# Performance work log

Measured on AMD Instinct MI355X. Metric: run time of the kernel, lower is better.

## Reference

```python
import jax, jax.numpy as jnp
import numpy as np
from jax import lax

DIM = 512
HEADS = 8
B, H, W = 8, 64, 64
EPS = 1e-12  # F.normalize default eps


def pointwise(x, w):
    # 1x1 conv, no bias: [B,C,H,W] x [O,C] -> [B,O,H,W]
    return jnp.einsum('oc,bchw->bohw', w, x)


def depthwise3x3(x, dw):
    # groups=C depthwise 3x3 conv, padding=1, no bias. dw: [C,1,3,3]
    return lax.conv_general_dilated(
        x, dw, window_strides=(1, 1), padding=((1, 1), (1, 1)),
        feature_group_count=x.shape[1],
        dimension_numbers=('NCHW', 'OIHW', 'NCHW'))


def setup_inputs() -> dict:
    key = jax.random.key(0)
    ks = jax.random.split(key, 8)
    s = 1.0 / np.sqrt(DIM)
    return {
        'x': jax.random.normal(ks[0], (B, DIM, H, W), jnp.float32),
        'w_q': jax.random.normal(ks[1], (DIM, DIM), jnp.float32) * s,
        'w_k': jax.random.normal(ks[2], (DIM, DIM), jnp.float32) * s,
        'w_v': jax.random.normal(ks[3], (DIM, DIM), jnp.float32) * s,
        'dw_q': jax.random.normal(ks[4], (DIM, 1, 3, 3), jnp.float32) * (1.0 / 3.0),
        'dw_k': jax.random.normal(ks[5], (DIM, 1, 3, 3), jnp.float32) * (1.0 / 3.0),
        'dw_v': jax.random.normal(ks[6], (DIM, 1, 3, 3), jnp.float32) * (1.0 / 3.0),
        'w_proj': jax.random.normal(ks[7], (DIM, DIM), jnp.float32) * s,
        'temperature': jnp.ones((HEADS, 1, 1), jnp.float32),
    }


def reference(x, w_q, w_k, w_v, dw_q, dw_k, dw_v, w_proj, temperature):
    b, c, h, w = x.shape
    d = c // HEADS
    hw = h * w

    q = depthwise3x3(pointwise(x, w_q), dw_q)
    k = depthwise3x3(pointwise(x, w_k), dw_k)
    v = depthwise3x3(pointwise(x, w_v), dw_v)

    # b (h d) x y -> b h d (x y)
    q = q.reshape(b, HEADS, d, hw)
    k = k.reshape(b, HEADS, d, hw)
    v = v.reshape(b, HEADS, d, hw)

    # L2-normalize over spatial axis (F.normalize, eps=1e-12)
    q = q / jnp.maximum(jnp.linalg.norm(q, axis=-1, keepdims=True), EPS)
    k = k / jnp.maximum(jnp.linalg.norm(k, axis=-1, keepdims=True), EPS)

    # channel attention: [b,h,d,d]
    attn = jnp.einsum('bhdn,bhen->bhde', q, k) * temperature
    attn = jax.nn.softmax(attn, axis=-1)
    out = jnp.einsum('bhde,bhen->bhdn', attn, v)  # [b,h,d,hw]

    out = out.reshape(b, c, h, w)
    return pointwise(out, w_proj)
```

## Files before the change

kernel.cpp:

```cpp
#include <hip/hip_runtime.h>
#include <hip/hip_bf16.h>
#include <stdint.h>

#define DEV __device__ __forceinline__

typedef __attribute__((ext_vector_type(8))) short   s16x8;
typedef __attribute__((ext_vector_type(8))) __bf16  bf16x8;
typedef __attribute__((ext_vector_type(4))) float   f32x4;

static constexpr int BATCH = 8;
static constexpr int DIM   = 512;
static constexpr int HEADS = 8;
static constexpr int HD    = 64;
static constexpr int HW    = 4096;
static constexpr int CQKV  = 1536;
static constexpr int NSPLIT = 8;

DEV void gload16(const void* g, void* l) {
  __builtin_amdgcn_global_load_lds(
      (const __attribute__((address_space(1))) void*)g,
      (__attribute__((address_space(3))) void*)l,
      16, 0, 0);
}

DEV f32x4 mfma16x32(s16x8 a, s16x8 b, f32x4 c) {
  return __builtin_amdgcn_mfma_f32_16x16x32_bf16(
      __builtin_bit_cast(bf16x8, a), __builtin_bit_cast(bf16x8, b), c, 0, 0, 0);
}

DEV float b2f(short x) {
  unsigned u = (unsigned)(unsigned short)x << 16;
  return __uint_as_float(u);
}
DEV short f2b(float f) { return __builtin_bit_cast(short, __float2bfloat16(f)); }

__global__ __launch_bounds__(256) void prep_weights(
    const float* __restrict__ wq, const float* __restrict__ wk,
    const float* __restrict__ wv, const float* __restrict__ wp,
    __hip_bfloat16* __restrict__ wqkv, __hip_bfloat16* __restrict__ wpb)
{
  int i = blockIdx.x * 256 + threadIdx.x;
  if (i < CQKV * DIM) {
    int r = i / DIM;
    const float* src = (r < 512) ? wq : (r < 1024) ? wk : wv;
    wqkv[i] = __float2bfloat16(src[(r & 511) * DIM + (i % DIM)]);
  } else {
    int j = i - CQKV * DIM;
    wpb[j] = __float2bfloat16(wp[j]);
  }
}

__global__ __launch_bounds__(256) void transpose_x(
    const float* __restrict__ x, __hip_bfloat16* __restrict__ XT)
{
  __shared__ float tile[64 * 65];
  const int n0 = blockIdx.x * 64, c0 = blockIdx.y * 64, b = blockIdx.z;
  const int t = threadIdx.x;
#pragma unroll
  for (int i = 0; i < 16; ++i) {
    int f = i * 256 + t; int ci = f >> 6, nj = f & 63;
    tile[ci * 65 + nj] = x[((long)b * DIM + c0 + ci) * HW + n0 + nj];
  }
  __syncthreads();
#pragma unroll
  for (int i = 0; i < 16; ++i) {
    int f = i * 256 + t; int ni = f >> 6, cj = f & 63;
    XT[((long)b * HW + n0 + ni) * DIM + c0 + cj] = __float2bfloat16(tile[cj * 65 + ni]);
  }
}

template <bool OUT_BF16>
__global__ __launch_bounds__(512, 2) void gemm_bt8(
    const __hip_bfloat16* __restrict__ A,
    const __hip_bfloat16* __restrict__ Bt,
    void* __restrict__ Cout,
    int M, int N, int K, long bt_bstride, long c_bstride)
{
  __shared__ __hip_bfloat16 lds[65536];
  const int t = threadIdx.x, w = t >> 6, l = t & 63;
  const int wm = w >> 2, wn = w & 3;
  const int m0 = blockIdx.y * 256, n0 = blockIdx.x * 256, b = blockIdx.z;
  const __hip_bfloat16* Bb = Bt + (long)b * bt_bstride;

  const int rl = t >> 3;
  const int ch = ((t & 7) ^ (rl & 7)) * 8;
  const int fr = l & 15, fk = (l >> 4) * 8;
  const int fswz = (l & 7) << 3;

  auto stageA = [&](int p, int h, int u) {
    const __hip_bfloat16* src = A + (long)(m0 + h * 64 + rl) * K + u * 64 + ch;
    __hip_bfloat16* dst = lds + p * 16384 + h * 8192 + w * 512;
    gload16(src, dst);
    gload16(src + 128l * K, dst + 4096);
  };
  auto stageB = [&](int p, int hb, int u) {
    const __hip_bfloat16* src = Bb + (long)(n0 + hb * 128 + rl) * K + u * 64 + ch;
    __hip_bfloat16* dst = lds + 32768 + p * 16384 + hb * 8192 + w * 512;
    gload16(src, dst);
    gload16(src + 64l * K, dst + 4096);
  };

  f32x4 acc[8][4] = {};
  const int NT = K >> 6;

  stageB(0, 0, 0); stageB(0, 1, 0); stageA(0, 0, 0); stageA(0, 1, 0);
  stageB(1, 0, 1); stageB(1, 1, 1); stageA(1, 0, 1);
  asm volatile("s_waitcnt vmcnt(6)" ::: "memory");
  __builtin_amdgcn_s_barrier();

  for (int u = 0; u < NT; ++u) {
    const int p = u & 1;
    const __hip_bfloat16* lA = lds + p * 16384 + wm * 4096;
    const __hip_bfloat16* lB = lds + 32768 + p * 16384 + (wn >> 1) * 8192
                             + (wn & 1) * 4096;
    s16x8 bfr[2][4];
#pragma unroll
    for (int q = 0; q < 4; ++q) {
      s16x8 afr[2][2];
#pragma unroll
      for (int kk = 0; kk < 2; ++kk)
#pragma unroll
        for (int mi = 0; mi < 2; ++mi)
          afr[kk][mi] = *(const s16x8*)&lA[(q >> 1) * 8192
              + ((q & 1) * 32 + mi * 16 + fr) * 64 + ((kk * 32 + fk) ^ fswz)];
      if (q == 0) {
#pragma unroll
        for (int kk = 0; kk < 2; ++kk)
#pragma unroll
          for (int ni = 0; ni < 4; ++ni)
            bfr[kk][ni] = *(const s16x8*)&lB[(ni * 16 + fr) * 64
                + ((kk * 32 + fk) ^ fswz)];
      }
      if (q == 0)      { if (u + 1 < NT) stageA(p ^ 1, 1, u + 1); }
      else if (q == 1) { if (u + 2 < NT) stageB(p, 0, u + 2); }
      else if (q == 2) { if (u + 2 < NT) stageB(p, 1, u + 2); }
      else {
        if (u + 2 < NT) stageA(p, 0, u + 2);
        if (u == NT - 2) asm volatile("s_waitcnt vmcnt(0)" ::: "memory");
        else             asm volatile("s_waitcnt vmcnt(6)" ::: "memory");
      }
      __builtin_amdgcn_s_barrier();
      asm volatile("s_waitcnt lgkmcnt(0)" ::: "memory");
      __builtin_amdgcn_sched_barrier(0);
      __builtin_amdgcn_s_setprio(1);
#pragma unroll
      for (int kk = 0; kk < 2; ++kk)
#pragma unroll
        for (int mi = 0; mi < 2; ++mi)
#pragma unroll
          for (int ni = 0; ni < 4; ++ni)
            acc[q * 2 + mi][ni] = mfma16x32(afr[kk][mi], bfr[kk][ni],
                                            acc[q * 2 + mi][ni]);
      __builtin_amdgcn_s_setprio(0);
      __builtin_amdgcn_s_barrier();
    }
  }

  const int row0 = m0 + wm * 128, col0 = n0 + wn * 64;
#pragma unroll
  for (int mi = 0; mi < 8; ++mi)
#pragma unroll
    for (int ni = 0; ni < 4; ++ni)
#pragma unroll
      for (int j = 0; j < 4; ++j) {
        long rr = row0 + mi * 16 + (l >> 4) * 4 + j;
        long cc = col0 + ni * 16 + fr;
        float v = acc[mi][ni][j];
        if (OUT_BF16)
          ((__hip_bfloat16*)Cout)[(long)b * c_bstride + rr * N + cc] = __float2bfloat16(v);
        else
          ((float*)Cout)[(long)b * c_bstride + rr * N + cc] = v;
      }
}

__global__ __launch_bounds__(256) void dwconv(
    __hip_bfloat16* __restrict__ P,
    const float* __restrict__ dwq, const float* __restrict__ dwk,
    const float* __restrict__ dwv, float* __restrict__ rnorm)
{
  __shared__ float pl[66 * 67];
  __shared__ float red4[4];
  const int c = blockIdx.x, b = blockIdx.y, t = threadIdx.x;
  const int w = t >> 6, l = t & 63;

  if (t < 66) { pl[t] = 0.f; pl[65 * 67 + t] = 0.f; }
  if (t >= 128 && t < 192) { pl[(t - 127) * 67] = 0.f; }
  if (t >= 192)            { pl[(t - 191) * 67 + 65] = 0.f; }

  const long base = ((long)b * CQKV + c) * HW;
  const int y = t >> 2, x0 = (t & 3) * 16;
  s16x8 v0 = *(const s16x8*)&P[base + t * 16];
  s16x8 v1 = *(const s16x8*)&P[base + t * 16 + 8];
#pragma unroll
  for (int j = 0; j < 8; ++j) {
    pl[(y + 1) * 67 + x0 + 1 + j] = b2f(v0[j]);
    pl[(y + 1) * 67 + x0 + 9 + j] = b2f(v1[j]);
  }
  __syncthreads();

  const int qkv = c >> 9, cc = c & 511;
  const float* dw = ((qkv == 0) ? dwq : (qkv == 1) ? dwk : dwv) + (long)cc * 9;
  const float w0 = dw[0], w1 = dw[1], w2 = dw[2], w3 = dw[3], w4 = dw[4],
              w5 = dw[5], w6 = dw[6], w7 = dw[7], w8 = dw[8];

  const float* r0 = &pl[y * 67 + x0];
  float outv[16];
  float ss = 0.f;
#pragma unroll
  for (int j = 0; j < 16; ++j) {
    float s = w0 * r0[j]       + w1 * r0[j + 1]   + w2 * r0[j + 2]
            + w3 * r0[j + 67]  + w4 * r0[j + 68]  + w5 * r0[j + 69]
            + w6 * r0[j + 134] + w7 * r0[j + 135] + w8 * r0[j + 136];
    outv[j] = s;
    ss += s * s;
  }
  s16x8 o0, o1;
#pragma unroll
  for (int j = 0; j < 8; ++j) { o0[j] = f2b(outv[j]); o1[j] = f2b(outv[j + 8]); }
  *(s16x8*)&P[base + t * 16]     = o0;
  *(s16x8*)&P[base + t * 16 + 8] = o1;

  if (qkv < 2) {
#pragma unroll
    for (int off = 32; off; off >>= 1) ss += __shfl_down(ss, off);
    if (l == 0) red4[w] = ss;
    __syncthreads();
    if (t == 0)
      rnorm[(long)b * 1024 + qkv * 512 + cc] =
          1.f / fmaxf(sqrtf(red4[0] + red4[1] + red4[2] + red4[3]), 1e-12f);
  }
}

__global__ __launch_bounds__(256) void transpose_v(
    const __hip_bfloat16* __restrict__ P, __hip_bfloat16* __restrict__ VT)
{
  __shared__ __hip_bfloat16 tile[64 * 65];
  const int n0 = blockIdx.x * 64, h = blockIdx.y, b = blockIdx.z;
  const int t = threadIdx.x;
#pragma unroll
  for (int i = 0; i < 16; ++i) {
    int f = i * 256 + t; int ei = f >> 6, nj = f & 63;
    tile[ei * 65 + nj] = P[((long)b * CQKV + 1024 + h * HD + ei) * HW + n0 + nj];
  }
  __syncthreads();
#pragma unroll
  for (int i = 0; i < 16; ++i) {
    int f = i * 256 + t; int ni = f >> 6, ej = f & 63;
    VT[(((long)b * HEADS + h) * HW + n0 + ni) * HD + ej] = tile[ej * 65 + ni];
  }
}

__global__ __launch_bounds__(256) void attn_partial(__hip_bfloat16* __restrict__ P)
{
  __shared__ __hip_bfloat16 ldsQ[64 * 128];
  __shared__ __hip_bfloat16 ldsK[64 * 128];
  const int t = threadIdx.x, w = t >> 6, l = t & 63;
  const int sp = blockIdx.x, h = blockIdx.y, b = blockIdx.z;
  const int wr = w >> 1, wc = w & 1;

  const long qbase = ((long)b * CQKV + h * HD) * HW;
  const long kbase = ((long)b * CQKV + 512 + h * HD) * HW;

  f32x4 acc[2][2] = {};

  const int kend = sp * 512 + 512;
  for (int k0 = sp * 512; k0 < kend; k0 += 128) {
#pragma unroll
    for (int i = 0; i < 4; ++i) {
      int r = w * 16 + i * 4 + (l >> 4);
      int c = (l & 15) ^ (r & 7);
      gload16(P + qbase + (long)r * HW + k0 + c * 8, &ldsQ[w * 2048 + i * 512]);
      gload16(P + kbase + (long)r * HW + k0 + c * 8, &ldsK[w * 2048 + i * 512]);
    }
    __syncthreads();
#pragma unroll
    for (int kk = 0; kk < 128; kk += 32) {
      s16x8 af[2], bfr[2];
#pragma unroll
      for (int mi = 0; mi < 2; ++mi) {
        int ar = wr * 32 + mi * 16 + (l & 15);
        int col = (kk + (l >> 4) * 8) ^ ((ar & 7) << 3);
        af[mi] = *(const s16x8*)&ldsQ[ar * 128 + col];
      }
#pragma unroll
      for (int ni = 0; ni < 2; ++ni) {
        int br = wc * 32 + ni * 16 + (l & 15);
        int col = (kk + (l >> 4) * 8) ^ ((br & 7) << 3);
        bfr[ni] = *(const s16x8*)&ldsK[br * 128 + col];
      }
#pragma unroll
      for (int mi = 0; mi < 2; ++mi)
#pragma unroll
        for (int ni = 0; ni < 2; ++ni)
          acc[mi][ni] = mfma16x32(af[mi], bfr[ni], acc[mi][ni]);
    }
    __syncthreads();
  }

  float* part = (float*)((char*)P + (long)b * (CQKV * HW * 2) + (1024l * HW * 2))
              + ((long)h * NSPLIT + sp) * 4096;
#pragma unroll
  for (int mi = 0; mi < 2; ++mi)
#pragma unroll
    for (int ni = 0; ni < 2; ++ni)
#pragma unroll
      for (int j = 0; j < 4; ++j) {
        int row = wr * 32 + mi * 16 + (l >> 4) * 4 + j;
        int col = wc * 32 + ni * 16 + (l & 15);
        part[row * 64 + col] = acc[mi][ni][j];
      }
}

__global__ __launch_bounds__(256) void attn_softmax(
    const __hip_bfloat16* __restrict__ P, const float* __restrict__ rnorm,
    const float* __restrict__ temp, __hip_bfloat16* __restrict__ attnb)
{
  __shared__ float S[64 * 65];
  const int t = threadIdx.x, h = blockIdx.x, b = blockIdx.y;
  const float* part = (const float*)((const char*)P + (long)b * (CQKV * HW * 2)
                                     + (1024l * HW * 2))
                    + (long)h * NSPLIT * 4096;
  const float tm = temp[h];

  for (int i = t; i < 4096; i += 256) {
    float s = 0.f;
#pragma unroll
    for (int p = 0; p < NSPLIT; ++p) s += part[p * 4096 + i];
    int r = i >> 6, c = i & 63;
    float rq = rnorm[(long)b * 1024 + h * HD + r];
    float rk = rnorm[(long)b * 1024 + 512 + h * HD + c];
    S[r * 65 + c] = s * rq * rk * tm;
  }
  __syncthreads();

  if (t < 64) {
    float m = -3.4e38f;
    for (int e = 0; e < 64; ++e) m = fmaxf(m, S[t * 65 + e]);
    float sum = 0.f;
    for (int e = 0; e < 64; ++e) {
      float ev = __expf(S[t * 65 + e] - m);
      S[t * 65 + e] = ev;
      sum += ev;
    }
    float inv = 1.f / sum;
    for (int e = 0; e < 64; ++e)
      attnb[(((long)b * HEADS + h) * 64 + t) * 64 + e] =
          __float2bfloat16(S[t * 65 + e] * inv);
  }
}

__global__ __launch_bounds__(256) void attn_apply_v(
    const __hip_bfloat16* __restrict__ VT, const __hip_bfloat16* __restrict__ attnb,
    __hip_bfloat16* __restrict__ OT)
{
  __shared__ __hip_bfloat16 ldsV[128 * 64];
  __shared__ __hip_bfloat16 ldsAt[64 * 64];
  const int t = threadIdx.x, w = t >> 6, l = t & 63;
  const int bh = blockIdx.y, b = bh >> 3, h = bh & 7;
  const int n0 = blockIdx.x * 128;

#pragma unroll
  for (int i = 0; i < 4; ++i) {
    int r = w * 32 + i * 8 + (l >> 3);
    int c = (l & 7) ^ (r & 7);
    gload16(VT + ((long)bh * HW + n0 + r) * HD + c * 8, &ldsV[w * 2048 + i * 512]);
  }
#pragma unroll
  for (int i = 0; i < 2; ++i) {
    int r = w * 16 + i * 8 + (l >> 3);
    int c = (l & 7) ^ (r & 7);
    gload16(attnb + ((long)bh * 64 + r) * 64 + c * 8, &ldsAt[w * 1024 + i * 512]);
  }
  __syncthreads();

  f32x4 acc[2][4] = {};
#pragma unroll
  for (int kk = 0; kk < 64; kk += 32) {
    s16x8 af[2], bfr[4];
#pragma unroll
    for (int mi = 0; mi < 2; ++mi) {
      int ar = w * 32 + mi * 16 + (l & 15);
      int col = (kk + (l >> 4) * 8) ^ ((ar & 7) << 3);
      af[mi] = *(const s16x8*)&ldsV[ar * 64 + col];
    }
#pragma unroll
    for (int ni = 0; ni < 4; ++ni) {
      int br = ni * 16 + (l & 15);
      int col = (kk + (l >> 4) * 8) ^ ((br & 7) << 3);
      bfr[ni] = *(const s16x8*)&ldsAt[br * 64 + col];
    }
#pragma unroll
    for (int mi = 0; mi < 2; ++mi)
#pragma unroll
      for (int ni = 0; ni < 4; ++ni)
        acc[mi][ni] = mfma16x32(af[mi], bfr[ni], acc[mi][ni]);
  }

#pragma unroll
  for (int mi = 0; mi < 2; ++mi)
#pragma unroll
    for (int ni = 0; ni < 4; ++ni)
#pragma unroll
      for (int j = 0; j < 4; ++j) {
        long n = n0 + w * 32 + mi * 16 + (l >> 4) * 4 + j;
        long c = h * HD + ni * 16 + (l & 15);
        OT[((long)b * HW + n) * DIM + c] = __float2bfloat16(acc[mi][ni][j]);
      }
}

extern "C" void kernel_launch(void* const* d_in, const int* in_sizes, int n_in,
                              void* d_out, int out_size, void* d_ws, size_t ws_size,
                              hipStream_t stream)
{
  const float* x    = (const float*)d_in[0];
  const float* wq   = (const float*)d_in[1];
  const float* wk   = (const float*)d_in[2];
  const float* wv   = (const float*)d_in[3];
  const float* dwq  = (const float*)d_in[4];
  const float* dwk  = (const float*)d_in[5];
  const float* dwv  = (const float*)d_in[6];
  const float* wp   = (const float*)d_in[7];
  const float* temp = (const float*)d_in[8];
  float* out = (float*)d_out;

  char* ws = (char*)d_ws;
  __hip_bfloat16* wqkv  = (__hip_bfloat16*)(ws + 0);
  __hip_bfloat16* wpb   = (__hip_bfloat16*)(ws + 1572864);
  float*          rnorm = (float*)(ws + 2097152);
  __hip_bfloat16* attnb = (__hip_bfloat16*)(ws + 2129920);
  __hip_bfloat16* XT    = (__hip_bfloat16*)(ws + (4l << 20));
  __hip_bfloat16* VT    = XT;
  __hip_bfloat16* P     = (__hip_bfloat16*)(ws + (40l << 20));
  __hip_bfloat16* OT    = P;

  prep_weights<<<4096, 256, 0, stream>>>(wq, wk, wv, wp, wqkv, wpb);
  transpose_x<<<dim3(64, 8, 8), 256, 0, stream>>>(x, XT);
  gemm_bt8<true><<<dim3(16, 6, 8), 512, 0, stream>>>(
      wqkv, XT, P, CQKV, HW, DIM, (long)HW * DIM, (long)CQKV * HW);
  dwconv<<<dim3(1536, 8), 256, 0, stream>>>(P, dwq, dwk, dwv, rnorm);
  transpose_v<<<dim3(64, 8, 8), 256, 0, stream>>>(P, VT);
  attn_partial<<<dim3(NSPLIT, 8, 8), 256, 0, stream>>>(P);
  attn_softmax<<<dim3(8, 8), 256, 0, stream>>>(P, rnorm, temp, attnb);
  attn_apply_v<<<dim3(32, 64), 256, 0, stream>>>(VT, attnb, OT);
  gemm_bt8<false><<<dim3(16, 2, 8), 512, 0, stream>>>(
      wpb, OT, out, DIM, HW, DIM, (long)HW * DIM, (long)DIM * HW);
}
```

Measured before the change: 193.7 us.

## Write V transposed from QKV GEMM epilogue and fuse V depthwise conv into transpose

The QKV projection now uses a new 128x128-tile GEMM whose epilogue writes the V channels directly in a per-head [n][e] layout. A new dwconv_vt kernel applies the V depthwise 3x3 conv on that transposed layout and writes VT, which removes the separate transpose_v pass and the V part of dwconv. The smaller GEMM tile replaces the 256x256 gemm_bt8 for this stage, which may lower per-block reuse. The V epilogue stores are 8-byte scattered writes, and the halo loads in dwconv_vt add some redundant traffic.

```diff
diff --git a/kernel.cpp b/kernel.cpp
--- a/kernel.cpp
+++ b/kernel.cpp
@@ -5,6 +5,7 @@
 #define DEV __device__ __forceinline__
 
 typedef __attribute__((ext_vector_type(8))) short   s16x8;
+typedef __attribute__((ext_vector_type(4))) short   s16x4;
 typedef __attribute__((ext_vector_type(8))) __bf16  bf16x8;
 typedef __attribute__((ext_vector_type(4))) float   f32x4;
 
@@ -66,6 +67,89 @@
   for (int i = 0; i < 16; ++i) {
     int f = i * 256 + t; int ni = f >> 6, cj = f & 63;
     XT[((long)b * HW + n0 + ni) * DIM + c0 + cj] = __float2bfloat16(tile[cj * 65 + ni]);
+  }
+}
+
+template <bool OUT_BF16>
+__global__ __launch_bounds__(256) void gemm_bt(
+    const __hip_bfloat16* __restrict__ A,
+    const __hip_bfloat16* __restrict__ Bt,
+    void* __restrict__ Cout,
+    int M, int N, int K, long bt_bstride, long c_bstride,
+    __hip_bfloat16* __restrict__ vt0)
+{
+  __shared__ __hip_bfloat16 ldsA[128 * 64];
+  __shared__ __hip_bfloat16 ldsB[128 * 64];
+  const int t = threadIdx.x, w = t >> 6, l = t & 63;
+  const int m0 = blockIdx.y * 128, n0 = blockIdx.x * 128, b = blockIdx.z;
+  const int wr = w >> 1, wc = w & 1;
+  const __hip_bfloat16* Bb = Bt + (long)b * bt_bstride;
+
+  f32x4 acc[4][4] = {};
+
+  for (int k0 = 0; k0 < K; k0 += 64) {
+#pragma unroll
+    for (int i = 0; i < 4; ++i) {
+      int r = w * 32 + i * 8 + (l >> 3);
+      int c = (l & 7) ^ (r & 7);
+      gload16(A  + (long)(m0 + r) * K + k0 + c * 8, &ldsA[w * 2048 + i * 512]);
+      gload16(Bb + (long)(n0 + r) * K + k0 + c * 8, &ldsB[w * 2048 + i * 512]);
+    }
+    __syncthreads();
+#pragma unroll
+    for (int kk = 0; kk < 64; kk += 32) {
+      s16x8 af[4], bfr[4];
+#pragma unroll
+      for (int mi = 0; mi < 4; ++mi) {
+        int ar = wr * 64 + mi * 16 + (l & 15);
+        int col = (kk + (l >> 4) * 8) ^ ((ar & 7) << 3);
+        af[mi] = *(const s16x8*)&ldsA[ar * 64 + col];
+      }
+#pragma unroll
+      for (int ni = 0; ni < 4; ++ni) {
+        int br = wc * 64 + ni * 16 + (l & 15);
+        int col = (kk + (l >> 4) * 8) ^ ((br & 7) << 3);
+        bfr[ni] = *(const s16x8*)&ldsB[br * 64 + col];
+      }
+#pragma unroll
+      for (int mi = 0; mi < 4; ++mi)
+#pragma unroll
+        for (int ni = 0; ni < 4; ++ni)
+          acc[mi][ni] = mfma16x32(af[mi], bfr[ni], acc[mi][ni]);
+    }
+    __syncthreads();
+  }
+
+  const int row0 = m0 + wr * 64, col0 = n0 + wc * 64;
+  if (vt0 != nullptr && row0 >= 1024) {
+    __hip_bfloat16* vbase = vt0 + (long)b * CQKV * HW + 1024l * HW;
+#pragma unroll
+    for (int mi = 0; mi < 4; ++mi)
+#pragma unroll
+      for (int ni = 0; ni < 4; ++ni) {
+        int ch = row0 - 1024 + mi * 16 + (l >> 4) * 4;
+        int hh = ch >> 6, e = ch & 63;
+        long cc = col0 + ni * 16 + (l & 15);
+        s16x4 pk;
+#pragma unroll
+        for (int j = 0; j < 4; ++j) pk[j] = f2b(acc[mi][ni][j]);
+        *(s16x4*)&vbase[(long)hh * (HW * 64l) + cc * 64 + e] = pk;
+      }
+  } else {
+#pragma unroll
+    for (int mi = 0; mi < 4; ++mi)
+#pragma unroll
+      for (int ni = 0; ni < 4; ++ni)
+#pragma unroll
+        for (int j = 0; j < 4; ++j) {
+          long rr = row0 + mi * 16 + (l >> 4) * 4 + j;
+          long cc = col0 + ni * 16 + (l & 15);
+          float v = acc[mi][ni][j];
+          if (OUT_BF16)
+            ((__hip_bfloat16*)Cout)[(long)b * c_bstride + rr * N + cc] = __float2bfloat16(v);
+          else
+            ((float*)Cout)[(long)b * c_bstride + rr * N + cc] = v;
+        }
   }
 }
 
@@ -176,7 +260,7 @@
 __global__ __launch_bounds__(256) void dwconv(
     __hip_bfloat16* __restrict__ P,
     const float* __restrict__ dwq, const float* __restrict__ dwk,
-    const float* __restrict__ dwv, float* __restrict__ rnorm)
+    float* __restrict__ rnorm)
 {
   __shared__ float pl[66 * 67];
   __shared__ float red4[4];
@@ -199,7 +283,7 @@
   __syncthreads();
 
   const int qkv = c >> 9, cc = c & 511;
-  const float* dw = ((qkv == 0) ? dwq : (qkv == 1) ? dwk : dwv) + (long)cc * 9;
+  const float* dw = ((qkv == 0) ? dwq : dwk) + (long)cc * 9;
   const float w0 = dw[0], w1 = dw[1], w2 = dw[2], w3 = dw[3], w4 = dw[4],
               w5 = dw[5], w6 = dw[6], w7 = dw[7], w8 = dw[8];
 
@@ -220,33 +304,78 @@
   *(s16x8*)&P[base + t * 16]     = o0;
   *(s16x8*)&P[base + t * 16 + 8] = o1;
 
-  if (qkv < 2) {
-#pragma unroll
-    for (int off = 32; off; off >>= 1) ss += __shfl_down(ss, off);
-    if (l == 0) red4[w] = ss;
-    __syncthreads();
-    if (t == 0)
-      rnorm[(long)b * 1024 + qkv * 512 + cc] =
-          1.f / fmaxf(sqrtf(red4[0] + red4[1] + red4[2] + red4[3]), 1e-12f);
-  }
-}
-
-__global__ __launch_bounds__(256) void transpose_v(
-    const __hip_bfloat16* __restrict__ P, __hip_bfloat16* __restrict__ VT)
-{
-  __shared__ __hip_bfloat16 tile[64 * 65];
-  const int n0 = blockIdx.x * 64, h = blockIdx.y, b = blockIdx.z;
-  const int t = threadIdx.x;
-#pragma unroll
-  for (int i = 0; i < 16; ++i) {
-    int f = i * 256 + t; int ei = f >> 6, nj = f & 63;
-    tile[ei * 65 + nj] = P[((long)b * CQKV + 1024 + h * HD + ei) * HW + n0 + nj];
-  }
+#pragma unroll
+  for (int off = 32; off; off >>= 1) ss += __shfl_down(ss, off);
+  if (l == 0) red4[w] = ss;
   __syncthreads();
-#pragma unroll
-  for (int i = 0; i < 16; ++i) {
-    int f = i * 256 + t; int ni = f >> 6, ej = f & 63;
-    VT[(((long)b * HEADS + h) * HW + n0 + ni) * HD + ej] = tile[ej * 65 + ni];
+  if (t == 0)
+    rnorm[(long)b * 1024 + qkv * 512 + cc] =
+        1.f / fmaxf(sqrtf(red4[0] + red4[1] + red4[2] + red4[3]), 1e-12f);
+}
+
+__global__ __launch_bounds__(256) void dwconv_vt(
+    const __hip_bfloat16* __restrict__ P,
+    const float* __restrict__ dwv,
+    __hip_bfloat16* __restrict__ VT)
+{
+  __shared__ __attribute__((aligned(16))) __hip_bfloat16 vb[416 * 64];
+  __shared__ float wlds[9][64];
+  const int t = threadIdx.x, w = t >> 6, l = t & 63;
+  const int s = blockIdx.x, h = blockIdx.y, b = blockIdx.z;
+  const int n0 = s * 256;
+  const __hip_bfloat16* VT0 = P + ((long)b * CQKV + 1024) * HW + (long)h * HW * 64;
+
+  if (t < 64) {
+#pragma unroll
+    for (int tap = 0; tap < 9; ++tap)
+      wlds[tap][t] = dwv[(h * 64 + t) * 9 + tap];
+  }
+  if (s == 0) {
+    s16x8 z = {};
+    for (int i = t; i < 80 * 8; i += 256) ((s16x8*)vb)[i] = z;
+  }
+  if (s == 15) {
+    s16x8 z = {};
+    for (int i = t; i < 80 * 8; i += 256) ((s16x8*)(vb + 336 * 64))[i] = z;
+  }
+#pragma unroll
+  for (int i = 0; i < 13; ++i) {
+    int R = i * 32 + w * 8 + (l >> 3);
+    int n = n0 - 80 + R;
+    if ((unsigned)n < (unsigned)HW)
+      gload16(VT0 + (long)n * 64 + (l & 7) * 8, vb + (i * 32 + w * 8) * 64);
+  }
+  __syncthreads();
+
+  const int cg = t & 7, ng = t >> 3;
+  float wreg[9][8];
+#pragma unroll
+  for (int tap = 0; tap < 9; ++tap)
+#pragma unroll
+    for (int j = 0; j < 8; ++j) wreg[tap][j] = wlds[tap][cg * 8 + j];
+
+  __hip_bfloat16* outp = VT + (((long)b * HEADS + h) * HW + n0 + ng * 8) * 64 + cg * 8;
+
+#pragma unroll
+  for (int y = 0; y < 8; ++y) {
+    const int rowc = 80 + ng * 8 + y;
+    const int x = (ng * 8 + y) & 63;
+    float accj[8] = {};
+#pragma unroll
+    for (int dy = 0; dy < 3; ++dy)
+#pragma unroll
+      for (int dx = 0; dx < 3; ++dx) {
+        if ((dx == 0 && x == 0) || (dx == 2 && x == 63)) continue;
+        const int tap = dy * 3 + dx;
+        const s16x8 v = *(const s16x8*)&vb[(rowc + (dy - 1) * 64 + (dx - 1)) * 64 + cg * 8];
+#pragma unroll
+        for (int j = 0; j < 8; ++j)
+          accj[j] = fmaf(wreg[tap][j], b2f(v[j]), accj[j]);
+      }
+    s16x8 o;
+#pragma unroll
+    for (int j = 0; j < 8; ++j) o[j] = f2b(accj[j]);
+    *(s16x8*)(outp + (long)y * 64) = o;
   }
 }
 
@@ -435,10 +564,10 @@
 
   prep_weights<<<4096, 256, 0, stream>>>(wq, wk, wv, wp, wqkv, wpb);
   transpose_x<<<dim3(64, 8, 8), 256, 0, stream>>>(x, XT);
-  gemm_bt8<true><<<dim3(16, 6, 8), 512, 0, stream>>>(
-      wqkv, XT, P, CQKV, HW, DIM, (long)HW * DIM, (long)CQKV * HW);
-  dwconv<<<dim3(1536, 8), 256, 0, stream>>>(P, dwq, dwk, dwv, rnorm);
-  transpose_v<<<dim3(64, 8, 8), 256, 0, stream>>>(P, VT);
+  gemm_bt<true><<<dim3(32, 12, 8), 256, 0, stream>>>(
+      wqkv, XT, P, CQKV, HW, DIM, (long)HW * DIM, (long)CQKV * HW, P);
+  dwconv<<<dim3(1024, 8), 256, 0, stream>>>(P, dwq, dwk, rnorm);
+  dwconv_vt<<<dim3(16, 8, 8), 256, 0, stream>>>(P, dwv, VT);
   attn_partial<<<dim3(NSPLIT, 8, 8), 256, 0, stream>>>(P);
   attn_softmax<<<dim3(8, 8), 256, 0, stream>>>(P, rnorm, temp, attnb);
   attn_apply_v<<<dim3(32, 64), 256, 0, stream>>>(VT, attnb, OT);
```

Measured after the change: 197.5 us. Within noise of the previous version (+2.0%).

## Add triple-buffered 128x128 GEMM kernel for QKV projection

Applied to the files above, without the earlier changes.

Adds a new GEMM kernel with 128x128 tiles, 256 threads and a three-stage LDS ring buffer. Global-to-LDS loads for tile u+2 are issued while MFMAs run on tile u, with vmcnt waits and barriers sequencing the stages. The QKV projection launch now uses this kernel with a larger grid (3072 blocks instead of 768), aiming for better latency hiding and occupancy. The trade-offs are less data reuse per block and scalar, uncoalesced epilogue stores.

```diff
diff --git a/kernel.cpp b/kernel.cpp
--- a/kernel.cpp
+++ b/kernel.cpp
@@ -67,6 +67,88 @@
     int f = i * 256 + t; int ni = f >> 6, cj = f & 63;
     XT[((long)b * HW + n0 + ni) * DIM + c0 + cj] = __float2bfloat16(tile[cj * 65 + ni]);
   }
+}
+
+template <bool OUT_BF16>
+__global__ __launch_bounds__(256) void gemm_pipe(
+    const __hip_bfloat16* __restrict__ A,
+    const __hip_bfloat16* __restrict__ Bt,
+    void* __restrict__ Cout,
+    int M, int N, int K, long bt_bstride, long c_bstride)
+{
+  __shared__ __hip_bfloat16 lds[24576];
+  const int t = threadIdx.x, w = t >> 6, l = t & 63;
+  const int wr = w >> 1, wc = w & 1;
+  const int m0 = blockIdx.y * 128, n0 = blockIdx.x * 128, b = blockIdx.z;
+  const __hip_bfloat16* Bb = Bt + (long)b * bt_bstride;
+
+  const int srow = t >> 2;
+  const int sch  = ((t & 3) ^ ((t >> 3) & 3)) * 8;
+  const __hip_bfloat16* a0 = A  + (long)(m0 + srow) * K + sch;
+  const __hip_bfloat16* b0 = Bb + (long)(n0 + srow) * K + sch;
+
+  auto stage = [&](int s, int u) {
+    const __hip_bfloat16* ap = a0 + u * 32;
+    const __hip_bfloat16* bp = b0 + u * 32;
+    __hip_bfloat16* d = lds + s * 8192 + t * 8;
+    gload16(ap,            d);
+    gload16(ap + 64l * K,  d + 2048);
+    gload16(bp,            d + 4096);
+    gload16(bp + 64l * K,  d + 6144);
+  };
+
+  const int fr = l & 15, g = l >> 4;
+  f32x4 acc[4][4] = {};
+  const int NT = K >> 5;
+
+  stage(0, 0);
+  stage(1, 1);
+
+  int s = 0;
+  for (int u = 0; u < NT; ++u) {
+    if (u < NT - 1) asm volatile("s_waitcnt vmcnt(4)" ::: "memory");
+    else            asm volatile("s_waitcnt vmcnt(0)" ::: "memory");
+    __builtin_amdgcn_s_barrier();
+    if (u + 2 < NT) stage(s == 0 ? 2 : s - 1, u + 2);
+
+    s16x8 af[4], bfr[4];
+#pragma unroll
+    for (int mi = 0; mi < 4; ++mi) {
+      int ar = wr * 64 + mi * 16 + fr;
+      af[mi] = *(const s16x8*)&lds[s * 8192 + ar * 32 + ((g ^ ((ar >> 1) & 3)) * 8)];
+    }
+#pragma unroll
+    for (int ni = 0; ni < 4; ++ni) {
+      int br = wc * 64 + ni * 16 + fr;
+      bfr[ni] = *(const s16x8*)&lds[s * 8192 + 4096 + br * 32 + ((g ^ ((br >> 1) & 3)) * 8)];
+    }
+    asm volatile("s_waitcnt lgkmcnt(0)" ::: "memory");
+    __builtin_amdgcn_sched_barrier(0);
+    __builtin_amdgcn_s_setprio(1);
+#pragma unroll
+    for (int mi = 0; mi < 4; ++mi)
+#pragma unroll
+      for (int ni = 0; ni < 4; ++ni)
+        acc[mi][ni] = mfma16x32(af[mi], bfr[ni], acc[mi][ni]);
+    __builtin_amdgcn_s_setprio(0);
+    s = (s == 2) ? 0 : s + 1;
+  }
+
+  const int row0 = m0 + wr * 64, col0 = n0 + wc * 64;
+#pragma unroll
+  for (int mi = 0; mi < 4; ++mi)
+#pragma unroll
+    for (int ni = 0; ni < 4; ++ni)
+#pragma unroll
+      for (int j = 0; j < 4; ++j) {
+        long rr = row0 + mi * 16 + (l >> 4) * 4 + j;
+        long cc = col0 + ni * 16 + (l & 15);
+        float v = acc[mi][ni][j];
+        if (OUT_BF16)
+          ((__hip_bfloat16*)Cout)[(long)b * c_bstride + rr * N + cc] = __float2bfloat16(v);
+        else
+          ((float*)Cout)[(long)b * c_bstride + rr * N + cc] = v;
+      }
 }
 
 template <bool OUT_BF16>
@@ -435,7 +517,7 @@
 
   prep_weights<<<4096, 256, 0, stream>>>(wq, wk, wv, wp, wqkv, wpb);
   transpose_x<<<dim3(64, 8, 8), 256, 0, stream>>>(x, XT);
-  gemm_bt8<true><<<dim3(16, 6, 8), 512, 0, stream>>>(
+  gemm_pipe<true><<<dim3(32, 12, 8), 256, 0, stream>>>(
       wqkv, XT, P, CQKV, HW, DIM, (long)HW * DIM, (long)CQKV * HW);
   dwconv<<<dim3(1536, 8), 256, 0, stream>>>(P, dwq, dwk, dwv, rnorm);
   transpose_v<<<dim3(64, 8, 8), 256, 0, stream>>>(P, VT);
```

Measured after the change: 196.8 us. No clear change (+1.6%).
